# Kernel optimization log

Measured on AMD Instinct MI355X. Metric: run time of the kernel, lower is better.

## Reference

```python
import jax, jax.numpy as jnp
import numpy as np

T, B, I, H, U = 256, 64, 512, 1024, 8  # time, batch, input, hidden, unit_input_size
EPS = 1e-5  # BatchNorm1d default eps


def setup_inputs() -> dict:
    key = jax.random.key(0)
    ks = jax.random.split(key, 8)
    x = jax.random.normal(ks[0], (T, B, I), dtype=jnp.float32)
    Wzx = jax.random.normal(ks[1], (H, I), dtype=jnp.float32) * (1.0 / np.sqrt(I))
    Whx = jax.random.normal(ks[2], (U * H, I), dtype=jnp.float32) * (np.sqrt(2.0 / I))
    Uz = jax.random.normal(ks[3], (H, H), dtype=jnp.float32) * (1.0 / np.sqrt(H))
    Uh = jax.random.normal(ks[4], (H, H), dtype=jnp.float32) * (1.0 / np.sqrt(H))
    b_unit = jnp.zeros((U * H,), dtype=jnp.float32)
    # block-diagonal matrix: row h has ones in columns [h*U, (h+1)*U)
    Wh_in_mask = jnp.kron(jnp.eye(H, dtype=jnp.float32), jnp.ones((1, U), dtype=jnp.float32))
    Wh_in = Wh_in_mask  # init value is exactly the block-diagonal ones matrix
    gz = jnp.ones((H,), dtype=jnp.float32)
    bz = jnp.zeros((H,), dtype=jnp.float32)
    gh = jnp.ones((H,), dtype=jnp.float32)
    bh = jnp.zeros((H,), dtype=jnp.float32)
    return {"x": x, "Wzx": Wzx, "Whx": Whx, "Uz": Uz, "Uh": Uh,
            "b_unit": b_unit, "Wh_in": Wh_in, "gz": gz, "bz": bz,
            "gh": gh, "bh": bh, "Wh_in_mask": Wh_in_mask}


def _bn(y, g, b):
    # training-mode BatchNorm1d: per-step batch stats over the batch dim, biased var
    mu = jnp.mean(y, axis=0)
    var = jnp.var(y, axis=0)
    return (y - mu) * jax.lax.rsqrt(var + EPS) * g + b


def reference(x, Wzx, Whx, Uz, Uh, b_unit, Wh_in, gz, bz, gh, bh, Wh_in_mask):
    # precompute input projections for all timesteps (math-equivalent, batched GEMM)
    zx = jnp.einsum('tbi,hi->tbh', x, Wzx)                 # [T,B,H]
    hx = jnp.einsum('tbi,ui->tbu', x, Whx) + b_unit        # [T,B,U*H]
    Wm = Wh_in * Wh_in_mask                                # [H,U*H] block-diag

    def step(h, inp):
        zx_t, hx_t = inp
        z = jax.nn.sigmoid(_bn(zx_t, gz, bz) + h @ Uz.T)           # [B,H]
        h_in = jax.nn.relu(hx_t)                                    # [B,U*H]
        h_ungated = jax.nn.relu(_bn(h_in @ Wm.T, gh, bh) + h @ Uh.T)
        h_new = z * h + (1.0 - z) * h_ungated
        return h_new, h_new

    h0 = jnp.zeros((x.shape[1], Uz.shape[0]), dtype=x.dtype)
    h_final, timeseries = jax.lax.scan(step, h0, (zx, hx))
    return timeseries, h_final
```

## Files before the change

### kernel.cpp

```cpp
#include <hip/hip_runtime.h>
#include <hip/hip_bf16.h>

#define T_DIM 256
#define B_DIM 64
#define I_DIM 512
#define H_DIM 1024
#define U_DIM 8
#define BN_EPS 1e-5f
#define BH (B_DIM * H_DIM)
#define NCHUNK 64
#define TILES_PER_CHUNK 80
#define NTILES 5120

typedef __bf16 bf16x8 __attribute__((ext_vector_type(8)));
typedef float f32x4 __attribute__((ext_vector_type(4)));
typedef int i32x4 __attribute__((ext_vector_type(4)));
typedef unsigned short u16;
typedef u16 u16x4 __attribute__((ext_vector_type(4)));
typedef unsigned long long u64;
using bf16 = __hip_bfloat16;


__global__ void k_cvt4(const float* __restrict__ in, u16* __restrict__ out, int n4) {
    int i = blockIdx.x * blockDim.x + threadIdx.x;
    int stride = gridDim.x * blockDim.x;
    for (; i < n4; i += stride) {
        f32x4 v = *reinterpret_cast<const f32x4*>(in + (size_t)i * 4);
        u16x4 o;
#pragma unroll
        for (int j = 0; j < 4; ++j)
            o[j] = __bfloat16_as_ushort(__float2bfloat16(v[j]));
        *reinterpret_cast<u16x4*>(out + (size_t)i * 4) = o;
    }
}

__global__ void k_pack_uzuh(const float* __restrict__ Uz, const float* __restrict__ Uh,
                            u16* __restrict__ out) {
    int i = blockIdx.x * 256 + threadIdx.x;
    int stride = gridDim.x * 256;
    int n4 = 2 * H_DIM * H_DIM / 4;
    for (; i < n4; i += stride) {
        int c = i * 4;
        int n = c >> 10, k = c & 1023;
        const float* src = (n < H_DIM) ? (Uz + (size_t)n * H_DIM + k)
                                       : (Uh + (size_t)(n - H_DIM) * H_DIM + k);
        f32x4 v = *reinterpret_cast<const f32x4*>(src);
        u16x4 o;
#pragma unroll
        for (int j = 0; j < 4; ++j)
            o[j] = __bfloat16_as_ushort(__float2bfloat16(v[j]));
        *reinterpret_cast<u16x4*>(out + c) = o;
    }
}

__global__ void k_wdiag(const float* __restrict__ Wh_in, const float* __restrict__ mask,
                        float* __restrict__ wdiag) {
    int idx = blockIdx.x * 256 + threadIdx.x;
    if (idx < H_DIM * U_DIM) {
        int h = idx >> 3;
        size_t col = (size_t)h * (H_DIM * U_DIM) + idx;
        wdiag[idx] = Wh_in[col] * mask[col];
    }
}

__device__ __forceinline__ bf16x8 cvt8(const float* p) {
    f32x4 a = *reinterpret_cast<const f32x4*>(p);
    f32x4 b = *reinterpret_cast<const f32x4*>(p + 4);
    union { u16 u[8]; bf16x8 v; } r;
#pragma unroll
    for (int j = 0; j < 4; ++j) {
        r.u[j]     = __bfloat16_as_ushort(__float2bfloat16(a[j]));
        r.u[4 + j] = __bfloat16_as_ushort(__float2bfloat16(b[j]));
    }
    return r.v;
}


__global__ __launch_bounds__(512, 2) void k_mega(
    const float* __restrict__ x,
    const bf16* __restrict__ wzx, const bf16* __restrict__ whx,
    const float* __restrict__ b_unit, const float* __restrict__ wdiag,
    const float* __restrict__ gzp, const float* __restrict__ bzp,
    const float* __restrict__ ghp, const float* __restrict__ bhp,
    const bf16* __restrict__ uzuh,
    bf16* bnz, bf16* bnh,
    bf16* hb0, bf16* hb1,
    float* out, unsigned* flags, unsigned* done) {

    __shared__ float smem[4096];
    int tid = threadIdx.x;

    if (blockIdx.x < 64) {
        int lane = tid & 63, w = tid >> 6;
        int cg = w >> 1, kq = w & 1;
        int r15 = lane & 15, kseg = lane >> 4;
        int cohort = blockIdx.x & 3, blk = blockIdx.x >> 2;
        int h0 = blk * 64 + cg * 16;
        int batch = cohort * 16 + r15;
        int hd0 = blk * 64 + cg * 16 + kseg * 4;

        bf16x8 aZ[16], aH[16];
        {
            const bf16* azb = uzuh + (size_t)(h0 + r15) * H_DIM + kq * 512 + kseg * 8;
            const bf16* ahb = azb + (size_t)H_DIM * H_DIM;
#pragma unroll
            for (int i = 0; i < 16; ++i) {
                aZ[i] = *reinterpret_cast<const bf16x8*>(azb + i * 32);
                aH[i] = *reinterpret_cast<const bf16x8*>(ahb + i * 32);
            }
        }

#define RED(zh, c, l, j) smem[(zh) * 1024 + (c) * 256 + (l) * 4 + (j)]

        f32x4 hreg = {};
        float bzv[4], bhv[4];

        for (int t = 0; t < T_DIM; ++t) {
            const bf16* hbc = (t & 1) ? hb1 : hb0;
            bf16* hbn = (t & 1) ? hb0 : hb1;

            if ((t & 3) == 0) {
                if (w == 0) {
                    while (__hip_atomic_load(&done[t >> 2], __ATOMIC_RELAXED,
                                             __HIP_MEMORY_SCOPE_AGENT) < (unsigned)TILES_PER_CHUNK)
                        __builtin_amdgcn_s_sleep(8);
                }
                __syncthreads();
                asm volatile("" ::: "memory");
                if (kq == 0) {
                    u16x4 vz = *reinterpret_cast<const u16x4*>(
                        bnz + (size_t)t * BH + (size_t)batch * H_DIM + hd0);
                    u16x4 vh = *reinterpret_cast<const u16x4*>(
                        bnh + (size_t)t * BH + (size_t)batch * H_DIM + hd0);
#pragma unroll
                    for (int j = 0; j < 4; ++j) {
                        bzv[j] = __bfloat162float(__ushort_as_bfloat16(vz[j]));
                        bhv[j] = __bfloat162float(__ushort_as_bfloat16(vh[j]));
                    }
                }
            }

            i32x4 hv[16];
            const bf16* hp = hbc + (size_t)batch * H_DIM + kq * 512 + kseg * 8;
#pragma unroll
            for (int i = 0; i < 16; ++i)
                asm volatile("global_load_dwordx4 %0, %1, off sc0 sc1"
                             : "=v"(hv[i]) : "v"(hp + i * 32));
            asm volatile("s_waitcnt vmcnt(0)" ::: "memory");
            __builtin_amdgcn_sched_barrier(0);

            f32x4 accZ = {}, accH = {};
#pragma unroll
            for (int i = 0; i < 16; ++i) {
                bf16x8 b = __builtin_bit_cast(bf16x8, hv[i]);
                accZ = __builtin_amdgcn_mfma_f32_16x16x32_bf16(aZ[i], b, accZ, 0, 0, 0);
                accH = __builtin_amdgcn_mfma_f32_16x16x32_bf16(aH[i], b, accH, 0, 0, 0);
            }

            if (kq == 1) {
                *reinterpret_cast<f32x4*>(&RED(0, cg, lane, 0)) = accZ;
                *reinterpret_cast<f32x4*>(&RED(1, cg, lane, 0)) = accH;
            }
            __syncthreads();

            if (kq == 0) {
                accZ += *reinterpret_cast<const f32x4*>(&RED(0, cg, lane, 0));
                accH += *reinterpret_cast<const f32x4*>(&RED(1, cg, lane, 0));
#pragma unroll
                for (int j = 0; j < 4; ++j) {
                    float z = 1.f / (1.f + __expf(-(bzv[j] + accZ[j])));
                    float hu = fmaxf(bhv[j] + accH[j], 0.f);
                    hreg[j] = z * hreg[j] + (1.f - z) * hu;
                }
                u16x4 o;
#pragma unroll
                for (int j = 0; j < 4; ++j)
                    o[j] = __bfloat16_as_ushort(__float2bfloat16(hreg[j]));
                u64 old = __hip_atomic_exchange(
                    (u64*)(hbn + (size_t)batch * H_DIM + hd0),
                    __builtin_bit_cast(u64, o),
                    __ATOMIC_RELAXED, __HIP_MEMORY_SCOPE_AGENT);
                asm volatile("" :: "v"(old));
            }

            if (t < T_DIM - 1) {
                __syncthreads();
                if (w == 0) {
                    if (lane == 0)
                        __hip_atomic_store(&flags[(size_t)(cohort * 16 + blk) * 16],
                                           (unsigned)(t + 1),
                                           __ATOMIC_RELAXED, __HIP_MEMORY_SCOPE_AGENT);
                    unsigned v;
                    do {
                        v = __hip_atomic_load(&flags[(size_t)(cohort * 16 + r15) * 16],
                                              __ATOMIC_RELAXED, __HIP_MEMORY_SCOPE_AGENT);
                        if (!__any(v <= (unsigned)t)) break;
                        __builtin_amdgcn_s_sleep(1);
                    } while (true);
                }
                __syncthreads();
            }

            if (kq == 0) {
                *reinterpret_cast<f32x4*>(out + (size_t)t * BH + (size_t)batch * H_DIM + hd0) = hreg;
                if (t == T_DIM - 1)
                    *reinterpret_cast<f32x4*>(out + (size_t)T_DIM * BH + (size_t)batch * H_DIM + hd0) = hreg;
                if (t + 1 < T_DIM && ((t + 1) & 3) != 0) {
                    u16x4 vz = *reinterpret_cast<const u16x4*>(
                        bnz + (size_t)(t + 1) * BH + (size_t)batch * H_DIM + hd0);
                    u16x4 vh = *reinterpret_cast<const u16x4*>(
                        bnh + (size_t)(t + 1) * BH + (size_t)batch * H_DIM + hd0);
#pragma unroll
                    for (int j = 0; j < 4; ++j) {
                        bzv[j] = __bfloat162float(__ushort_as_bfloat16(vz[j]));
                        bhv[j] = __bfloat162float(__ushort_as_bfloat16(vh[j]));
                    }
                }
            }
        }
        return;
    }

    {
        int q = blockIdx.x - 64;
        int sub = tid >> 8;
        int ltid = tid & 255;
        int lane = ltid & 63;
        int mq = ltid >> 6;
        int r15 = lane & 15;
        int kseg = lane >> 4;
        float* sm = smem + sub * 2048;
#define SB(st, wd, tt, col) sm[(st) * 1024 + (wd) * 256 + (tt) * 64 + (col)]

        for (int g = q * 2 + sub; g < NTILES; g += 384) {
            int c = g / TILES_PER_CHUNK;
            int s = g % TILES_PER_CHUNK;
            int t0 = c * 4;

            if (s < 16) {
                int h0 = s * 64;
                const float* xbase = x + (size_t)(t0 * B_DIM + mq * 16 + r15) * I_DIM + kseg * 8;
                f32x4 acc[4][4] = {};
                for (int kk = 0; kk < I_DIM; kk += 32) {
                    bf16x8 b[4];
#pragma unroll
                    for (int nf = 0; nf < 4; ++nf)
                        b[nf] = *reinterpret_cast<const bf16x8*>(
                            wzx + (size_t)(h0 + nf * 16 + r15) * I_DIM + kk + kseg * 8);
#pragma unroll
                    for (int tt = 0; tt < 4; ++tt) {
                        bf16x8 a = cvt8(xbase + (size_t)tt * B_DIM * I_DIM + kk);
#pragma unroll
                        for (int nf = 0; nf < 4; ++nf)
                            acc[tt][nf] = __builtin_amdgcn_mfma_f32_16x16x32_bf16(
                                a, b[nf], acc[tt][nf], 0, 0, 0);
                    }
                }
#pragma unroll
                for (int tt = 0; tt < 4; ++tt)
#pragma unroll
                    for (int nf = 0; nf < 4; ++nf) {
                        float sv = acc[tt][nf][0] + acc[tt][nf][1] + acc[tt][nf][2] + acc[tt][nf][3];
                        float s2 = acc[tt][nf][0] * acc[tt][nf][0] + acc[tt][nf][1] * acc[tt][nf][1] +
                                   acc[tt][nf][2] * acc[tt][nf][2] + acc[tt][nf][3] * acc[tt][nf][3];
                        sv += __shfl_xor(sv, 16); sv += __shfl_xor(sv, 32);
                        s2 += __shfl_xor(s2, 16); s2 += __shfl_xor(s2, 32);
                        if (lane < 16) {
                            SB(0, mq, tt, nf * 16 + r15) = sv;
                            SB(1, mq, tt, nf * 16 + r15) = s2;
                        }
                    }
                __syncthreads();
                int bb = mq * 16 + kseg * 4;
#pragma unroll
                for (int tt = 0; tt < 4; ++tt)
#pragma unroll
                    for (int nf = 0; nf < 4; ++nf) {
                        int col = nf * 16 + r15;
                        float sv = SB(0, 0, tt, col) + SB(0, 1, tt, col) + SB(0, 2, tt, col) + SB(0, 3, tt, col);
                        float s2 = SB(1, 0, tt, col) + SB(1, 1, tt, col) + SB(1, 2, tt, col) + SB(1, 3, tt, col);
                        float mu = sv * (1.f / B_DIM);
                        float var = s2 * (1.f / B_DIM) - mu * mu;
                        int h = h0 + col;
                        float sc = rsqrtf(var + BN_EPS) * gzp[h];
                        float sh = bzp[h] - mu * sc;
#pragma unroll
                        for (int j = 0; j < 4; ++j)
                            bnz[(size_t)((t0 + tt) * B_DIM + bb + j) * H_DIM + h] =
                                __float2bfloat16(acc[tt][nf][j] * sc + sh);
                    }
            } else {
                int h0 = (s - 16) * 16;
                int u0 = h0 * U_DIM;
                const float* xbase = x + (size_t)(t0 * B_DIM + mq * 16 + r15) * I_DIM + kseg * 8;
                f32x4 acc[4][8] = {};
                for (int kk = 0; kk < I_DIM; kk += 32) {
                    bf16x8 b[8];
#pragma unroll
                    for (int nf = 0; nf < 8; ++nf)
                        b[nf] = *reinterpret_cast<const bf16x8*>(
                            whx + (size_t)(u0 + nf * 16 + r15) * I_DIM + kk + kseg * 8);
#pragma unroll
                    for (int tt = 0; tt < 4; ++tt) {
                        bf16x8 a = cvt8(xbase + (size_t)tt * B_DIM * I_DIM + kk);
#pragma unroll
                        for (int nf = 0; nf < 8; ++nf)
                            acc[tt][nf] = __builtin_amdgcn_mfma_f32_16x16x32_bf16(
                                a, b[nf], acc[tt][nf], 0, 0, 0);
                    }
                }
                int uloc = r15 & 7;
#pragma unroll
                for (int nf = 0; nf < 8; ++nf) {
                    int ucol = u0 + nf * 16 + r15;
                    float wd = wdiag[ucol];
                    float bu = b_unit[ucol];
#pragma unroll
                    for (int tt = 0; tt < 4; ++tt)
#pragma unroll
                        for (int j = 0; j < 4; ++j) {
                            float v = fmaxf(acc[tt][nf][j] + bu, 0.f) * wd;
                            v += __shfl_xor(v, 1);
                            v += __shfl_xor(v, 2);
                            v += __shfl_xor(v, 4);
                            acc[tt][nf][j] = v;
                        }
                }
#pragma unroll
                for (int tt = 0; tt < 4; ++tt)
#pragma unroll
                    for (int nf = 0; nf < 8; ++nf) {
                        float sv = 0.f, s2 = 0.f;
                        if (uloc == 0) {
#pragma unroll
                            for (int j = 0; j < 4; ++j) {
                                sv += acc[tt][nf][j];
                                s2 += acc[tt][nf][j] * acc[tt][nf][j];
                            }
                        }
                        sv += __shfl_xor(sv, 16); sv += __shfl_xor(sv, 32);
                        s2 += __shfl_xor(s2, 16); s2 += __shfl_xor(s2, 32);
                        if (lane == 0 || lane == 8) {
                            int col = nf * 2 + (r15 >> 3);
                            SB(0, mq, tt, col) = sv;
                            SB(1, mq, tt, col) = s2;
                        }
                    }
                __syncthreads();
                int bb = mq * 16 + kseg * 4;
#pragma unroll
                for (int tt = 0; tt < 4; ++tt)
#pragma unroll
                    for (int nf = 0; nf < 8; ++nf) {
                        int col = nf * 2 + (r15 >> 3);
                        float sv = SB(0, 0, tt, col) + SB(0, 1, tt, col) + SB(0, 2, tt, col) + SB(0, 3, tt, col);
                        float s2 = SB(1, 0, tt, col) + SB(1, 1, tt, col) + SB(1, 2, tt, col) + SB(1, 3, tt, col);
                        float mu = sv * (1.f / B_DIM);
                        float var = s2 * (1.f / B_DIM) - mu * mu;
                        int h = h0 + col;
                        float sc = rsqrtf(var + BN_EPS) * ghp[h];
                        float sh = bhp[h] - mu * sc;
                        if (uloc == 0) {
#pragma unroll
                            for (int j = 0; j < 4; ++j)
                                bnh[(size_t)((t0 + tt) * B_DIM + bb + j) * H_DIM + h] =
                                    __float2bfloat16(acc[tt][nf][j] * sc + sh);
                        }
                    }
            }
            __syncthreads();
            if (ltid == 0)
                __hip_atomic_fetch_add(&done[c], 1u, __ATOMIC_RELEASE, __HIP_MEMORY_SCOPE_AGENT);
        }
    }
}

#define OFF_WZX   ((size_t)16777216)
#define OFF_WHX   ((size_t)17825792)
#define OFF_UZUH  ((size_t)26214400)
#define OFF_WDIAG ((size_t)30408704)
#define OFF_BNZ   ((size_t)30441472)
#define OFF_BNH   ((size_t)63995904)
#define OFF_BAR   ((size_t)97550336)
#define OFF_DONE  ((size_t)97615872)
#define OFF_HB0   ((size_t)98074624)
#define OFF_HB1   ((size_t)98205696)

extern "C" void kernel_launch(void* const* d_in, const int* in_sizes, int n_in,
                              void* d_out, int out_size, void* d_ws, size_t ws_size,
                              hipStream_t stream) {
    const float* x      = (const float*)d_in[0];
    const float* Wzx    = (const float*)d_in[1];
    const float* Whx    = (const float*)d_in[2];
    const float* Uz     = (const float*)d_in[3];
    const float* Uh     = (const float*)d_in[4];
    const float* b_unit = (const float*)d_in[5];
    const float* Wh_in  = (const float*)d_in[6];
    const float* gz     = (const float*)d_in[7];
    const float* bz     = (const float*)d_in[8];
    const float* gh     = (const float*)d_in[9];
    const float* bh     = (const float*)d_in[10];
    const float* mask   = (const float*)d_in[11];

    char* ws = (char*)d_ws;
    bf16*     wzx_b = (bf16*)(ws + OFF_WZX);
    bf16*     whx_b = (bf16*)(ws + OFF_WHX);
    bf16*     uzuh  = (bf16*)(ws + OFF_UZUH);
    float*    wdiag = (float*)(ws + OFF_WDIAG);
    bf16*     bnz   = (bf16*)(ws + OFF_BNZ);
    bf16*     bnh   = (bf16*)(ws + OFF_BNH);
    unsigned* flags = (unsigned*)(ws + OFF_BAR);
    unsigned* done  = (unsigned*)(ws + OFF_DONE);
    bf16*     hb0   = (bf16*)(ws + OFF_HB0);
    bf16*     hb1   = (bf16*)(ws + OFF_HB1);

    float* out = (float*)d_out;

    k_cvt4<<<512, 256, 0, stream>>>(Wzx, (u16*)wzx_b, H_DIM * I_DIM / 4);
    k_cvt4<<<2048, 256, 0, stream>>>(Whx, (u16*)whx_b, U_DIM * H_DIM * I_DIM / 4);
    k_pack_uzuh<<<2048, 256, 0, stream>>>(Uz, Uh, (u16*)uzuh);
    k_wdiag<<<(H_DIM * U_DIM + 255) / 256, 256, 0, stream>>>(Wh_in, mask, wdiag);

    hipMemsetAsync(hb0, 0, (size_t)BH * sizeof(bf16), stream);
    hipMemsetAsync(flags, 0, 4096, stream);
    hipMemsetAsync(done, 0, 4096, stream);

    k_mega<<<256, 512, 0, stream>>>(x, wzx_b, whx_b, b_unit, wdiag,
                                    gz, bz, gh, bh, uzuh,
                                    bnz, bnh, hb0, hb1, out, flags, done);
}
```

Baseline: 1.806 ms.

## Replace per-block barrier with per-wave dependency flags in recurrent loop

The recurrent loop now synchronises at wave granularity. Each column-group wave publishes its own progress flag after writing its slice of h. Each wave then polls only the 32 flags covering the half of h it reads, where before every wave waited on a block-wide barrier across all blocks in the cohort. The LDS reduction buffer is double-buffered by timestep parity so one __syncthreads can be dropped, and the flag region is enlarged to match. The intent is to shorten the critical path of each timestep. The risk is memory-ordering subtleties with relaxed atomics and more polling traffic.

```diff
diff --git a/kernel.cpp b/kernel.cpp
--- a/kernel.cpp
+++ b/kernel.cpp
@@ -99,6 +99,10 @@
         int batch = cohort * 16 + r15;
         int hd0 = blk * 64 + cg * 16 + kseg * 4;
 
+        unsigned* fbase = flags + (size_t)cohort * 1024;
+        unsigned* myflag = fbase + (size_t)(blk * 4 + cg) * 16;
+        unsigned* depflag = fbase + (size_t)(kq * 32 + (lane & 31)) * 16;
+
         bf16x8 aZ[16], aH[16];
         {
             const bf16* azb = uzuh + (size_t)(h0 + r15) * H_DIM + kq * 512 + kseg * 8;
@@ -110,7 +114,7 @@
             }
         }
 
-#define RED(zh, c, l, j) smem[(zh) * 1024 + (c) * 256 + (l) * 4 + (j)]
+#define REDX(par, zh, c, l, j) smem[(par) * 2048 + (zh) * 1024 + (c) * 256 + (l) * 4 + (j)]
 
         f32x4 hreg = {};
         float bzv[4], bhv[4];
@@ -119,24 +123,28 @@
             const bf16* hbc = (t & 1) ? hb1 : hb0;
             bf16* hbn = (t & 1) ? hb0 : hb1;
 
-            if ((t & 3) == 0) {
-                if (w == 0) {
-                    while (__hip_atomic_load(&done[t >> 2], __ATOMIC_RELAXED,
-                                             __HIP_MEMORY_SCOPE_AGENT) < (unsigned)TILES_PER_CHUNK)
-                        __builtin_amdgcn_s_sleep(8);
-                }
-                __syncthreads();
+            if ((t & 3) == 0 && kq == 0) {
+                while (__hip_atomic_load(&done[t >> 2], __ATOMIC_RELAXED,
+                                         __HIP_MEMORY_SCOPE_AGENT) < (unsigned)TILES_PER_CHUNK)
+                    __builtin_amdgcn_s_sleep(8);
                 asm volatile("" ::: "memory");
-                if (kq == 0) {
-                    u16x4 vz = *reinterpret_cast<const u16x4*>(
-                        bnz + (size_t)t * BH + (size_t)batch * H_DIM + hd0);
-                    u16x4 vh = *reinterpret_cast<const u16x4*>(
-                        bnh + (size_t)t * BH + (size_t)batch * H_DIM + hd0);
-#pragma unroll
-                    for (int j = 0; j < 4; ++j) {
-                        bzv[j] = __bfloat162float(__ushort_as_bfloat16(vz[j]));
-                        bhv[j] = __bfloat162float(__ushort_as_bfloat16(vh[j]));
-                    }
+                u16x4 vz = *reinterpret_cast<const u16x4*>(
+                    bnz + (size_t)t * BH + (size_t)batch * H_DIM + hd0);
+                u16x4 vh = *reinterpret_cast<const u16x4*>(
+                    bnh + (size_t)t * BH + (size_t)batch * H_DIM + hd0);
+#pragma unroll
+                for (int j = 0; j < 4; ++j) {
+                    bzv[j] = __bfloat162float(__ushort_as_bfloat16(vz[j]));
+                    bhv[j] = __bfloat162float(__ushort_as_bfloat16(vh[j]));
+                }
+            }
+
+            if (t > 0) {
+                while (true) {
+                    unsigned v = __hip_atomic_load(depflag, __ATOMIC_RELAXED,
+                                                   __HIP_MEMORY_SCOPE_AGENT);
+                    if (!__any(v < (unsigned)t)) break;
+                    __builtin_amdgcn_s_sleep(1);
                 }
             }
 
@@ -157,51 +165,37 @@
                 accH = __builtin_amdgcn_mfma_f32_16x16x32_bf16(aH[i], b, accH, 0, 0, 0);
             }
 
+            int par = t & 1;
             if (kq == 1) {
-                *reinterpret_cast<f32x4*>(&RED(0, cg, lane, 0)) = accZ;
-                *reinterpret_cast<f32x4*>(&RED(1, cg, lane, 0)) = accH;
+                *reinterpret_cast<f32x4*>(&REDX(par, 0, cg, lane, 0)) = accZ;
+                *reinterpret_cast<f32x4*>(&REDX(par, 1, cg, lane, 0)) = accH;
             }
             __syncthreads();
 
             if (kq == 0) {
-                accZ += *reinterpret_cast<const f32x4*>(&RED(0, cg, lane, 0));
-                accH += *reinterpret_cast<const f32x4*>(&RED(1, cg, lane, 0));
+                accZ += *reinterpret_cast<const f32x4*>(&REDX(par, 0, cg, lane, 0));
+                accH += *reinterpret_cast<const f32x4*>(&REDX(par, 1, cg, lane, 0));
 #pragma unroll
                 for (int j = 0; j < 4; ++j) {
                     float z = 1.f / (1.f + __expf(-(bzv[j] + accZ[j])));
                     float hu = fmaxf(bhv[j] + accH[j], 0.f);
                     hreg[j] = z * hreg[j] + (1.f - z) * hu;
                 }
-                u16x4 o;
-#pragma unroll
-                for (int j = 0; j < 4; ++j)
-                    o[j] = __bfloat16_as_ushort(__float2bfloat16(hreg[j]));
-                u64 old = __hip_atomic_exchange(
-                    (u64*)(hbn + (size_t)batch * H_DIM + hd0),
-                    __builtin_bit_cast(u64, o),
-                    __ATOMIC_RELAXED, __HIP_MEMORY_SCOPE_AGENT);
-                asm volatile("" :: "v"(old));
-            }
-
-            if (t < T_DIM - 1) {
-                __syncthreads();
-                if (w == 0) {
+                if (t < T_DIM - 1) {
+                    u16x4 o;
+#pragma unroll
+                    for (int j = 0; j < 4; ++j)
+                        o[j] = __bfloat16_as_ushort(__float2bfloat16(hreg[j]));
+                    u64 old = __hip_atomic_exchange(
+                        (u64*)(hbn + (size_t)batch * H_DIM + hd0),
+                        __builtin_bit_cast(u64, o),
+                        __ATOMIC_RELAXED, __HIP_MEMORY_SCOPE_AGENT);
+                    asm volatile("" :: "v"(old));
+                    asm volatile("s_waitcnt vmcnt(0)" ::: "memory");
                     if (lane == 0)
-                        __hip_atomic_store(&flags[(size_t)(cohort * 16 + blk) * 16],
-                                           (unsigned)(t + 1),
+                        __hip_atomic_store(myflag, (unsigned)(t + 1),
                                            __ATOMIC_RELAXED, __HIP_MEMORY_SCOPE_AGENT);
-                    unsigned v;
-                    do {
-                        v = __hip_atomic_load(&flags[(size_t)(cohort * 16 + r15) * 16],
-                                              __ATOMIC_RELAXED, __HIP_MEMORY_SCOPE_AGENT);
-                        if (!__any(v <= (unsigned)t)) break;
-                        __builtin_amdgcn_s_sleep(1);
-                    } while (true);
-                }
-                __syncthreads();
-            }
-
-            if (kq == 0) {
+                }
                 *reinterpret_cast<f32x4*>(out + (size_t)t * BH + (size_t)batch * H_DIM + hd0) = hreg;
                 if (t == T_DIM - 1)
                     *reinterpret_cast<f32x4*>(out + (size_t)T_DIM * BH + (size_t)batch * H_DIM + hd0) = hreg;
@@ -422,7 +416,7 @@
     k_wdiag<<<(H_DIM * U_DIM + 255) / 256, 256, 0, stream>>>(Wh_in, mask, wdiag);
 
     hipMemsetAsync(hb0, 0, (size_t)BH * sizeof(bf16), stream);
-    hipMemsetAsync(flags, 0, 4096, stream);
+    hipMemsetAsync(flags, 0, 16384, stream);
     hipMemsetAsync(done, 0, 4096, stream);
 
     k_mega<<<256, 512, 0, stream>>>(x, wzx_b, whx_b, b_unit, wdiag,
```

Measured after the change: 1.918 ms. +6.2%, slower.
